# Optimization experiments

Hardware: AMD Instinct MI355X
Metric: run time of the kernel (lower is better)

The kernel has to match this reference:

```python
import jax, jax.numpy as jnp
import numpy as np

N_NODES = 100000
N_EDGES = 3200000
N_FEAT = 128
N_GRAPHS = 512
BN_EPS = 1e-5


def setup_inputs() -> dict:
    key = jax.random.key(0)
    ks = jax.random.split(key, 16)
    x = jax.random.normal(ks[0], (N_NODES, N_FEAT), dtype=jnp.float32)
    edge_index = jax.random.randint(ks[1], (2, N_EDGES), 0, N_NODES, dtype=jnp.int32)
    batch = jnp.sort(jax.random.randint(ks[2], (N_NODES,), 0, N_GRAPHS, dtype=jnp.int32))
    def lin(k, fi, fo):
        s = 1.0 / np.sqrt(fi)
        return jax.random.uniform(k, (fi, fo), jnp.float32, -s, s)
    return {
        "x": x,
        "edge_index": edge_index,
        "batch": batch,
        # conv1: GraphConv(128 -> 30): lin_rel (with bias) + lin_root (no bias)
        "W_rel1": lin(ks[3], N_FEAT, 30),
        "W_root1": lin(ks[4], N_FEAT, 30),
        "b1": jnp.zeros((30,), jnp.float32),
        "bn1_g": jnp.ones((30,), jnp.float32),
        "bn1_b": jnp.zeros((30,), jnp.float32),
        "bn1_m": jnp.zeros((30,), jnp.float32),
        "bn1_v": jnp.ones((30,), jnp.float32),
        # conv2: GraphConv(30 -> 20)
        "W_rel2": lin(ks[5], 30, 20),
        "W_root2": lin(ks[6], 30, 20),
        "b2": jnp.zeros((20,), jnp.float32),
        "bn2_g": jnp.ones((20,), jnp.float32),
        "bn2_b": jnp.zeros((20,), jnp.float32),
        "bn2_m": jnp.zeros((20,), jnp.float32),
        "bn2_v": jnp.ones((20,), jnp.float32),
        # head
        "W_lin1": lin(ks[7], 40, 10),
        "b_lin1": jnp.zeros((10,), jnp.float32),
        "W_lin2": lin(ks[8], 10, 1),
        "b_lin2": jnp.zeros((1,), jnp.float32),
    }


def _bn(h, g, b, m, v):
    return (h - m) * jax.lax.rsqrt(v + BN_EPS) * g + b


def reference(x, edge_index, batch,
              W_rel1, W_root1, b1, bn1_g, bn1_b, bn1_m, bn1_v,
              W_rel2, W_root2, b2, bn2_g, bn2_b, bn2_m, bn2_v,
              W_lin1, b_lin1, W_lin2, b_lin2):
    n = x.shape[0]
    src, dst = edge_index[0], edge_index[1]
    # ---- GraphConv 1: out = aggr_add(x_src -> dst) @ W_rel + x @ W_root + b
    agg = jax.ops.segment_sum(x[src], dst, num_segments=n)  # [N,128]
    h = jax.nn.relu(agg @ W_rel1 + x @ W_root1 + b1)        # [N,30]
    h = _bn(h, bn1_g, bn1_b, bn1_m, bn1_v)
    # ---- GraphConv 2
    agg2 = jax.ops.segment_sum(h[src], dst, num_segments=n)  # [N,30]
    h2 = jax.nn.relu(agg2 @ W_rel2 + h @ W_root2 + b2)       # [N,20]
    h2 = _bn(h2, bn2_g, bn2_b, bn2_m, bn2_v)
    # ---- global pools over graph ids
    gmax = jax.ops.segment_max(h2, batch, num_segments=N_GRAPHS)  # [G,20]
    gmax = jnp.where(jnp.isfinite(gmax), gmax, 0.0)
    gsum = jax.ops.segment_sum(h2, batch, num_segments=N_GRAPHS)
    cnt = jax.ops.segment_sum(jnp.ones((n,), h2.dtype), batch, num_segments=N_GRAPHS)
    gmean = gsum / jnp.maximum(cnt, 1.0)[:, None]
    z = jnp.concatenate([gmax, gmean], axis=1)               # [G,40]
    z = jax.nn.relu(z @ W_lin1 + b_lin1)
    return jax.nn.sigmoid(z @ W_lin2 + b_lin2)               # [G,1]
```

## Files before the change

kernel.cpp:

```cpp
#include <hip/hip_runtime.h>
#include <math.h>

#define NFEAT 128
#define F1    30
#define F1P   32
#define F2    20

#define EPB   8192
#define BW    512
#define EDCAP 9216

__global__ __launch_bounds__(256) void k_prepw(
    const float* __restrict__ Wrel, const float* __restrict__ Wroot,
    float* __restrict__ Wp)
{
    int i = blockIdx.x * 256 + threadIdx.x;
    if (i >= 2 * 128 * 32) return;
    int table = i >> 12, rem = i & 4095, k = rem >> 5, j = rem & 31;
    const float* W = table ? Wroot : Wrel;
    Wp[i] = (j < F1) ? W[k * F1 + j] : 0.f;
}

__global__ __launch_bounds__(512) void k_proj1(
    const float* __restrict__ x, const float* __restrict__ Wp,
    float* __restrict__ y1, float* __restrict__ r1, int n)
{
    __shared__ float4 xs4[2048];
    int tid = threadIdx.x;
    int base = blockIdx.x * 64;

#pragma unroll
    for (int it = 0; it < 4; it++) {
        int idx = it * 512 + tid;
        int k4 = idx & 31, row = idx >> 5;
        int gnode = base + row;
        float4 v = make_float4(0.f, 0.f, 0.f, 0.f);
        if (gnode < n) v = ((const float4*)(x + (size_t)gnode * NFEAT))[k4];
        xs4[k4 * 64 + (row ^ k4)] = v;
    }
    __syncthreads();

    int lane = tid & 63;
    int combo = __builtin_amdgcn_readfirstlane(tid >> 6);
    int table = combo >> 2, q = combo & 3;
    int node = base + lane;
    if (node >= n) return;

    const float* Wt = Wp + table * 4096 + q * 8;
    float acc[8];
#pragma unroll
    for (int j = 0; j < 8; j++) acc[j] = 0.f;

    for (int k4 = 0; k4 < 32; k4++) {
        float4 xk = xs4[k4 * 64 + (lane ^ k4)];
#pragma unroll
        for (int kk = 0; kk < 4; kk++) {
            float xs = kk == 0 ? xk.x : kk == 1 ? xk.y : kk == 2 ? xk.z : xk.w;
            const float* w = Wt + (k4 * 4 + kk) * 32;
            acc[0] += xs * w[0]; acc[1] += xs * w[1];
            acc[2] += xs * w[2]; acc[3] += xs * w[3];
            acc[4] += xs * w[4]; acc[5] += xs * w[5];
            acc[6] += xs * w[6]; acc[7] += xs * w[7];
        }
    }
    float* outp = (table ? r1 : y1) + (size_t)node * F1P + q * 8;
    ((float4*)outp)[0] = make_float4(acc[0], acc[1], acc[2], acc[3]);
    ((float4*)outp)[1] = make_float4(acc[4], acc[5], acc[6], acc[7]);
}

__global__ __launch_bounds__(512) void k_p1(
    const int* __restrict__ ei, int* __restrict__ blockCnt,
    int E, int nbuck)
{
    __shared__ int lh[256];
    int t = threadIdx.x;
    for (int i = t; i < 256; i += 512) lh[i] = 0;
    __syncthreads();
    const int* dst = ei + E;
    int base = blockIdx.x * EPB;
#pragma unroll 4
    for (int k = 0; k < EPB / 512; k++) {
        int e = base + k * 512 + t;
        if (e < E) atomicAdd(&lh[dst[e] >> 9], 1);
    }
    __syncthreads();
    int* out = blockCnt + (size_t)blockIdx.x * nbuck;
    for (int i = t; i < nbuck; i += 512) out[i] = lh[i];
}

__global__ __launch_bounds__(256) void k_p2(
    const int* __restrict__ blockCnt, int* __restrict__ blockOff,
    int* __restrict__ bucketTot, int neb, int nbuck)
{
    __shared__ int sdata[256];
    __shared__ int carry_s;
    int b = blockIdx.x;
    int t = threadIdx.x;
    if (t == 0) carry_s = 0;
    __syncthreads();
    for (int base = 0; base < neb; base += 512) {
        int i0 = base + 2 * t, i1 = i0 + 1;
        int c0 = (i0 < neb) ? blockCnt[(size_t)i0 * nbuck + b] : 0;
        int c1 = (i1 < neb) ? blockCnt[(size_t)i1 * nbuck + b] : 0;
        int s = c0 + c1;
        sdata[t] = s;
        __syncthreads();
        for (int off = 1; off < 256; off <<= 1) {
            int tmp = (t >= off) ? sdata[t - off] : 0;
            __syncthreads();
            sdata[t] += tmp;
            __syncthreads();
        }
        int ex = carry_s + sdata[t] - s;
        if (i0 < neb) blockOff[(size_t)i0 * nbuck + b] = ex;
        if (i1 < neb) blockOff[(size_t)i1 * nbuck + b] = ex + c0;
        __syncthreads();
        if (t == 255) carry_s += sdata[255];
        __syncthreads();
    }
    if (t == 0) bucketTot[b] = carry_s;
}

__global__ __launch_bounds__(256) void k_p3(
    const int* __restrict__ bucketTot, int* __restrict__ bucketStart, int nbuck)
{
    __shared__ int sdata[256];
    int t = threadIdx.x;
    int v[4]; int s = 0;
#pragma unroll
    for (int i = 0; i < 4; i++) {
        int idx = t * 4 + i;
        v[i] = (idx < nbuck) ? bucketTot[idx] : 0;
        s += v[i];
    }
    sdata[t] = s;
    __syncthreads();
    for (int off = 1; off < 256; off <<= 1) {
        int tmp = (t >= off) ? sdata[t - off] : 0;
        __syncthreads();
        sdata[t] += tmp;
        __syncthreads();
    }
    int ex = sdata[t] - s;
#pragma unroll
    for (int i = 0; i < 4; i++) {
        int idx = t * 4 + i;
        if (idx < nbuck) bucketStart[idx] = ex;
        ex += v[i];
    }
    if (t == 255) bucketStart[nbuck] = sdata[255];
}

__global__ __launch_bounds__(512) void k_p4(
    const int* __restrict__ ei, const int* __restrict__ bucketStart,
    const int* __restrict__ blockOff, int* __restrict__ ebuf,
    int E, int nbuck)
{
    __shared__ int cur[256];
    int t = threadIdx.x;
    const int* boff = blockOff + (size_t)blockIdx.x * nbuck;
    for (int i = t; i < nbuck; i += 512) cur[i] = bucketStart[i] + boff[i];
    __syncthreads();
    const int* dst = ei + E;
    int base = blockIdx.x * EPB;
#pragma unroll 4
    for (int k = 0; k < EPB / 512; k++) {
        int e = base + k * 512 + t;
        if (e < E) {
            int s = ei[e], d = dst[e];
            int p = atomicAdd(&cur[d >> 9], 1);
            ebuf[p] = (s << 9) | (d & 511);
        }
    }
}

__global__ __launch_bounds__(512) void k_p6(
    const int* __restrict__ ebuf, const int* __restrict__ bucketStart,
    int* __restrict__ perm, int* __restrict__ deg, int* __restrict__ rowstart,
    int n, int t1, int t2, int t3)
{
    __shared__ int ed2[EDCAP];
    __shared__ int hist[1024];
    __shared__ int sdata[512];
    __shared__ int m0_s;
    int t = threadIdx.x;
    int b = blockIdx.x >> 1;
    int h = blockIdx.x & 1;
    int lo = bucketStart[b], hi = bucketStart[b + 1];
    hist[t] = 0; hist[t + 512] = 0;
    if (t == 0) m0_s = 0;
    __syncthreads();

    int c0 = 0;
    for (int p = lo + t; p < hi; p += 512) {
        int e = ebuf[p];
        int dl9 = e & 511;
        if ((dl9 >> 8) == 0) c0++;
        if ((dl9 >> 8) == h) {
            int src = e >> 9;
            int qq = (src >= t1) + (src >= t2) + (src >= t3);
            atomicAdd(&hist[(dl9 & 255) * 4 + qq], 1);
        }
    }
    atomicAdd(&m0_s, c0);
    __syncthreads();

    int v0 = hist[2 * t], v1 = hist[2 * t + 1];
    int ps = v0 + v1;
    sdata[t] = ps;
    __syncthreads();
    for (int off = 1; off < 512; off <<= 1) {
        int tmp = (t >= off) ? sdata[t - off] : 0;
        __syncthreads();
        sdata[t] += tmp;
        __syncthreads();
    }
    int ex = sdata[t] - ps;
    hist[2 * t] = ex;
    hist[2 * t + 1] = ex + v0;
    __syncthreads();
    int mh = sdata[511];
    int base = lo + (h ? m0_s : 0);

    if (t < 256) {
        int node = b * BW + h * 256 + t;
        if (node < n) {
            int s0 = hist[t * 4];
            int s1 = (t == 255) ? mh : hist[(t + 1) * 4];
            deg[node] = s1 - s0;
            rowstart[node] = base + s0;
        }
    }
    __syncthreads();

    for (int p = lo + t; p < hi; p += 512) {
        int e = ebuf[p];
        int dl9 = e & 511;
        if ((dl9 >> 8) == h) {
            int src = e >> 9;
            int qq = (src >= t1) + (src >= t2) + (src >= t3);
            int pos = atomicAdd(&hist[(dl9 & 255) * 4 + qq], 1);
            if (pos < EDCAP) ed2[pos] = src;
            else perm[base + pos] = src;
        }
    }
    __syncthreads();

    int mw = min(mh, EDCAP);
    for (int i = t; i < mw; i += 512) perm[base + i] = ed2[i];
}

__global__ __launch_bounds__(256) void k_agg1(
    const int* __restrict__ rowstart, const int* __restrict__ deg,
    const int* __restrict__ perm, const float* __restrict__ y1,
    float* __restrict__ agg1, int n)
{
    int idx = blockIdx.x * 256 + threadIdx.x;
    int node = idx >> 3, q = idx & 7;
    if (node >= n) return;
    int s = rowstart[node], e = s + deg[node];
    float4 acc = {0.f, 0.f, 0.f, 0.f};
    int j = s;
    for (; j + 8 <= e; j += 8) {
        int myp = perm[j + q];
#pragma unroll
        for (int k = 0; k < 8; k++) {
            int sr = __shfl(myp, k, 8);
            float4 v = *(const float4*)(y1 + (size_t)sr * F1P + q * 4);
            acc.x += v.x; acc.y += v.y; acc.z += v.z; acc.w += v.w;
        }
    }
    for (; j < e; j++) {
        int sr = perm[j];
        float4 v = *(const float4*)(y1 + (size_t)sr * F1P + q * 4);
        acc.x += v.x; acc.y += v.y; acc.z += v.z; acc.w += v.w;
    }
    *(float4*)(agg1 + (size_t)node * F1P + q * 4) = acc;
}

__global__ __launch_bounds__(256) void k_agg2(
    const int* __restrict__ rowstart, const int* __restrict__ deg,
    const int* __restrict__ perm, const float* __restrict__ y2,
    float* __restrict__ agg2, int n)
{
    int idx = blockIdx.x * 256 + threadIdx.x;
    int node = idx >> 3, q = idx & 7;
    if (node >= n) return;
    bool valid = (q < 5);
    int s = rowstart[node], e = s + deg[node];
    float4 acc = {0.f, 0.f, 0.f, 0.f};
    int j = s;
    for (; j + 8 <= e; j += 8) {
        int myp = perm[j + q];
#pragma unroll
        for (int k = 0; k < 8; k++) {
            int sr = __shfl(myp, k, 8);
            if (valid) {
                float4 v = *(const float4*)(y2 + (size_t)sr * F2 + q * 4);
                acc.x += v.x; acc.y += v.y; acc.z += v.z; acc.w += v.w;
            }
        }
    }
    if (valid) {
        for (; j < e; j++) {
            int sr = perm[j];
            float4 v = *(const float4*)(y2 + (size_t)sr * F2 + q * 4);
            acc.x += v.x; acc.y += v.y; acc.z += v.z; acc.w += v.w;
        }
        *(float4*)(agg2 + (size_t)node * F2 + q * 4) = acc;
    }
}

__global__ __launch_bounds__(256) void k_mid(
    const float* __restrict__ agg1, const float* __restrict__ r1,
    const float* __restrict__ b1,
    const float* __restrict__ g1, const float* __restrict__ bb1,
    const float* __restrict__ m1, const float* __restrict__ v1,
    const float* __restrict__ Wrel2, const float* __restrict__ Wroot2,
    const float* __restrict__ b2,
    float* __restrict__ y2, float* __restrict__ r2, int n)
{
    int node = blockIdx.x * 256 + threadIdx.x;
    if (node >= n) return;
    float h[F1];
    const float4* av = (const float4*)(agg1 + (size_t)node * F1P);
    const float4* rv = (const float4*)(r1   + (size_t)node * F1P);
#pragma unroll
    for (int q = 0; q < 8; q++) {
        float4 a = av[q], r = rv[q];
        int j = q * 4;
        if (j + 0 < F1) h[j + 0] = a.x + r.x;
        if (j + 1 < F1) h[j + 1] = a.y + r.y;
        if (j + 2 < F1) h[j + 2] = a.z + r.z;
        if (j + 3 < F1) h[j + 3] = a.w + r.w;
    }
#pragma unroll
    for (int j = 0; j < F1; j++) {
        float t = fmaxf(h[j] + b1[j], 0.f);
        float sc = g1[j] / sqrtf(v1[j] + 1e-5f);
        h[j] = (t - m1[j]) * sc + bb1[j];
    }
    float ay[F2], ar[F2];
#pragma unroll
    for (int j = 0; j < F2; j++) { ay[j] = 0.f; ar[j] = b2[j]; }
    for (int k = 0; k < F1; k++) {
        float hk = h[k];
#pragma unroll
        for (int j = 0; j < F2; j++) {
            ay[j] += hk * Wrel2 [k * F2 + j];
            ar[j] += hk * Wroot2[k * F2 + j];
        }
    }
    float4* yo = (float4*)(y2 + (size_t)node * F2);
    float4* ro = (float4*)(r2 + (size_t)node * F2);
#pragma unroll
    for (int q = 0; q < 5; q++) {
        float4 vy, vr;
        vy.x = ay[q*4+0]; vy.y = ay[q*4+1]; vy.z = ay[q*4+2]; vy.w = ay[q*4+3];
        vr.x = ar[q*4+0]; vr.y = ar[q*4+1]; vr.z = ar[q*4+2]; vr.w = ar[q*4+3];
        yo[q] = vy;  ro[q] = vr;
    }
}

__global__ __launch_bounds__(256) void k_pool(
    const float* __restrict__ agg2, const float* __restrict__ r2,
    const int* __restrict__ batch,
    const float* __restrict__ g2, const float* __restrict__ bb2,
    const float* __restrict__ m2, const float* __restrict__ v2,
    unsigned* __restrict__ gmaxU, float* __restrict__ gsum,
    int* __restrict__ cnt, int n)
{
    int t = threadIdx.x;
    if (t >= 240) return;
    int i = t / 20, j = t - (t / 20) * 20;
    int base = blockIdx.x * 256;
    int nend = min(base + 256, n);
    float sc = g2[j] / sqrtf(v2[j] + 1e-5f);
    float mj = m2[j], bj = bb2[j];

    int curg = -1, c = 0;
    float mx = -3.4e38f, sm = 0.f;
    for (int node = base + i; node < nend; node += 12) {
        int g = batch[node];
        if (g != curg) {
            if (curg >= 0) {
                atomicAdd(&gsum[curg * F2 + j], sm);
                unsigned bits = __float_as_uint(mx);
                unsigned mapped = (bits & 0x80000000u) ? ~bits : (bits | 0x80000000u);
                atomicMax(&gmaxU[curg * F2 + j], mapped);
                if (j == 0) atomicAdd(&cnt[curg], c);
            }
            curg = g; c = 0; mx = -3.4e38f; sm = 0.f;
        }
        float a = agg2[(size_t)node * F2 + j] + r2[(size_t)node * F2 + j];
        a = fmaxf(a, 0.f);
        float h2 = (a - mj) * sc + bj;
        mx = fmaxf(mx, h2); sm += h2; c++;
    }
    if (curg >= 0) {
        atomicAdd(&gsum[curg * F2 + j], sm);
        unsigned bits = __float_as_uint(mx);
        unsigned mapped = (bits & 0x80000000u) ? ~bits : (bits | 0x80000000u);
        atomicMax(&gmaxU[curg * F2 + j], mapped);
        if (j == 0) atomicAdd(&cnt[curg], c);
    }
}

__global__ __launch_bounds__(256) void k_head(
    const unsigned* __restrict__ gmaxU, const float* __restrict__ gsum,
    const int* __restrict__ cnt,
    const float* __restrict__ W1, const float* __restrict__ b1h,
    const float* __restrict__ W2, const float* __restrict__ b2h,
    float* __restrict__ out, int G)
{
    int g = blockIdx.x * 256 + threadIdx.x;
    if (g >= G) return;
    int c = cnt[g];
    float cf = fmaxf((float)c, 1.f);
    float z[2 * F2];
#pragma unroll
    for (int j = 0; j < F2; j++) {
        unsigned u = gmaxU[g * F2 + j];
        float gm = 0.f;
        if (c != 0) {
            gm = (u & 0x80000000u) ? __uint_as_float(u & 0x7FFFFFFFu)
                                   : __uint_as_float(~u);
            if (!isfinite(gm)) gm = 0.f;
        }
        z[j]      = gm;
        z[F2 + j] = gsum[g * F2 + j] / cf;
    }
    float a[10];
#pragma unroll
    for (int i = 0; i < 10; i++) a[i] = b1h[i];
    for (int k = 0; k < 2 * F2; k++) {
        float zk = z[k];
#pragma unroll
        for (int i = 0; i < 10; i++) a[i] += zk * W1[k * 10 + i];
    }
    float o = b2h[0];
#pragma unroll
    for (int i = 0; i < 10; i++) o += fmaxf(a[i], 0.f) * W2[i];
    out[g] = 1.f / (1.f + expf(-o));
}

extern "C" void kernel_launch(void* const* d_in, const int* in_sizes, int n_in,
                              void* d_out, int out_size, void* d_ws, size_t ws_size,
                              hipStream_t stream)
{
    const float* x      = (const float*)d_in[0];
    const int*   ei     = (const int*)  d_in[1];
    const int*   batch  = (const int*)  d_in[2];
    const float* Wrel1  = (const float*)d_in[3];
    const float* Wroot1 = (const float*)d_in[4];
    const float* b1     = (const float*)d_in[5];
    const float* bn1_g  = (const float*)d_in[6];
    const float* bn1_b  = (const float*)d_in[7];
    const float* bn1_m  = (const float*)d_in[8];
    const float* bn1_v  = (const float*)d_in[9];
    const float* Wrel2  = (const float*)d_in[10];
    const float* Wroot2 = (const float*)d_in[11];
    const float* b2     = (const float*)d_in[12];
    const float* bn2_g  = (const float*)d_in[13];
    const float* bn2_b  = (const float*)d_in[14];
    const float* bn2_m  = (const float*)d_in[15];
    const float* bn2_v  = (const float*)d_in[16];
    const float* W_lin1 = (const float*)d_in[17];
    const float* b_lin1 = (const float*)d_in[18];
    const float* W_lin2 = (const float*)d_in[19];
    const float* b_lin2 = (const float*)d_in[20];
    float* out = (float*)d_out;

    int n = in_sizes[0] / NFEAT;
    int E = in_sizes[1] / 2;
    int G = out_size;
    int nbuck = (n + BW - 1) / BW;
    int neb = (E + EPB - 1) / EPB;
    int qs = (n + 3) >> 2;

    char* p = (char*)d_ws;
    float* y1   = (float*)p;  p += (size_t)n * F1P * 4;
    float* r1   = (float*)p;  p += (size_t)n * F1P * 4;
    char* alias0 = p;
    float* agg1 = (float*)p;  p += (size_t)n * F1P * 4;
    float* y2   = (float*)p;  p += (size_t)n * F2 * 4;
    float* r2   = (float*)p;  p += (size_t)n * F2 * 4;
    char* alias1 = p;
    float* agg2 = (float*)p;  p += (size_t)n * F2 * 4;
    unsigned* gmaxU = (unsigned*)p;  p += (size_t)G * F2 * 4;
    float*    gsum  = (float*)p;     p += (size_t)G * F2 * 4;
    int*      cnt   = (int*)p;       p += (size_t)G * 4;
    int* deg      = (int*)p;  p += (size_t)n * 4;
    int* rowstart = (int*)p;  p += (size_t)n * 4;
    int* perm     = (int*)p;  p += (size_t)E * 4;
    float* Wp     = (float*)p; p += 2 * 128 * 32 * 4;

    int* ebuf = (int*)alias0;
    int* blockCnt    = (int*)alias1;
    int* blockOff    = blockCnt + (size_t)neb * nbuck;
    int* bucketTot   = blockOff + (size_t)neb * nbuck;
    int* bucketStart = bucketTot + nbuck;

    hipMemsetAsync(gmaxU, 0, (size_t)G * (F2 * 4 * 2 + 4), stream);

    k_p1<<<neb, 512, 0, stream>>>(ei, blockCnt, E, nbuck);
    k_p2<<<nbuck, 256, 0, stream>>>(blockCnt, blockOff, bucketTot, neb, nbuck);
    k_p3<<<1, 256, 0, stream>>>(bucketTot, bucketStart, nbuck);
    k_p4<<<neb, 512, 0, stream>>>(ei, bucketStart, blockOff, ebuf, E, nbuck);
    k_p6<<<nbuck * 2, 512, 0, stream>>>(ebuf, bucketStart, perm, deg, rowstart, n,
                                        qs, 2 * qs, 3 * qs);

    k_prepw<<<32, 256, 0, stream>>>(Wrel1, Wroot1, Wp);
    k_proj1<<<(n + 63) / 64, 512, 0, stream>>>(x, Wp, y1, r1, n);
    k_agg1<<<((size_t)n * 8 + 255) / 256, 256, 0, stream>>>(rowstart, deg, perm, y1, agg1, n);
    k_mid<<<(n + 255) / 256, 256, 0, stream>>>(agg1, r1, b1, bn1_g, bn1_b, bn1_m,
                                               bn1_v, Wrel2, Wroot2, b2, y2, r2, n);
    k_agg2<<<((size_t)n * 8 + 255) / 256, 256, 0, stream>>>(rowstart, deg, perm, y2, agg2, n);
    k_pool<<<(n + 255) / 256, 256, 0, stream>>>(agg2, r2, batch, bn2_g, bn2_b,
                                                bn2_m, bn2_v, gmaxU, gsum, cnt, n);
    k_head<<<(G + 255) / 256, 256, 0, stream>>>(gmaxU, gsum, cnt, W_lin1, b_lin1,
                                                W_lin2, b_lin2, out, G);
}
```

Baseline: 389.2 us.

## Fuse layer-1 aggregation with mid MLP and layer-2 aggregation with pooling

Merges the first neighbor aggregation with the BN/ReLU and second projection into one kernel using shared memory, and merges the second aggregation with BN and graph pooling. This removes the agg1/agg2 intermediate buffers and two launches, avoiding global round-trips of the aggregated features. The workspace layout is reorganized so ebuf and the bucket counters no longer alias the removed buffers. Pooling now runs serially on 20 threads per 32-node block, which issues more atomics per graph than the old 256-node blocks.

Result: faster. 366.5 us (-5.8%).

```diff
diff --git a/kernel.cpp b/kernel.cpp
--- a/kernel.cpp
+++ b/kernel.cpp
@@ -250,159 +250,200 @@
     for (int i = t; i < mw; i += 512) perm[base + i] = ed2[i];
 }
 
-__global__ __launch_bounds__(256) void k_agg1(
+__global__ __launch_bounds__(256) void k_agg1m(
     const int* __restrict__ rowstart, const int* __restrict__ deg,
     const int* __restrict__ perm, const float* __restrict__ y1,
-    float* __restrict__ agg1, int n)
-{
-    int idx = blockIdx.x * 256 + threadIdx.x;
-    int node = idx >> 3, q = idx & 7;
-    if (node >= n) return;
-    int s = rowstart[node], e = s + deg[node];
-    float4 acc = {0.f, 0.f, 0.f, 0.f};
-    int j = s;
-    for (; j + 8 <= e; j += 8) {
-        int myp = perm[j + q];
-#pragma unroll
-        for (int k = 0; k < 8; k++) {
-            int sr = __shfl(myp, k, 8);
-            float4 v = *(const float4*)(y1 + (size_t)sr * F1P + q * 4);
-            acc.x += v.x; acc.y += v.y; acc.z += v.z; acc.w += v.w;
-        }
-    }
-    for (; j < e; j++) {
-        int sr = perm[j];
-        float4 v = *(const float4*)(y1 + (size_t)sr * F1P + q * 4);
-        acc.x += v.x; acc.y += v.y; acc.z += v.z; acc.w += v.w;
-    }
-    *(float4*)(agg1 + (size_t)node * F1P + q * 4) = acc;
-}
-
-__global__ __launch_bounds__(256) void k_agg2(
-    const int* __restrict__ rowstart, const int* __restrict__ deg,
-    const int* __restrict__ perm, const float* __restrict__ y2,
-    float* __restrict__ agg2, int n)
-{
-    int idx = blockIdx.x * 256 + threadIdx.x;
-    int node = idx >> 3, q = idx & 7;
-    if (node >= n) return;
-    bool valid = (q < 5);
-    int s = rowstart[node], e = s + deg[node];
-    float4 acc = {0.f, 0.f, 0.f, 0.f};
-    int j = s;
-    for (; j + 8 <= e; j += 8) {
-        int myp = perm[j + q];
-#pragma unroll
-        for (int k = 0; k < 8; k++) {
-            int sr = __shfl(myp, k, 8);
-            if (valid) {
-                float4 v = *(const float4*)(y2 + (size_t)sr * F2 + q * 4);
-                acc.x += v.x; acc.y += v.y; acc.z += v.z; acc.w += v.w;
-            }
-        }
-    }
-    if (valid) {
-        for (; j < e; j++) {
-            int sr = perm[j];
-            float4 v = *(const float4*)(y2 + (size_t)sr * F2 + q * 4);
-            acc.x += v.x; acc.y += v.y; acc.z += v.z; acc.w += v.w;
-        }
-        *(float4*)(agg2 + (size_t)node * F2 + q * 4) = acc;
-    }
-}
-
-__global__ __launch_bounds__(256) void k_mid(
-    const float* __restrict__ agg1, const float* __restrict__ r1,
-    const float* __restrict__ b1,
-    const float* __restrict__ g1, const float* __restrict__ bb1,
-    const float* __restrict__ m1, const float* __restrict__ v1,
+    const float* __restrict__ r1,
+    const float* __restrict__ b1, const float* __restrict__ g1,
+    const float* __restrict__ bb1, const float* __restrict__ m1,
+    const float* __restrict__ v1,
     const float* __restrict__ Wrel2, const float* __restrict__ Wroot2,
     const float* __restrict__ b2,
     float* __restrict__ y2, float* __restrict__ r2, int n)
 {
-    int node = blockIdx.x * 256 + threadIdx.x;
-    if (node >= n) return;
-    float h[F1];
-    const float4* av = (const float4*)(agg1 + (size_t)node * F1P);
-    const float4* rv = (const float4*)(r1   + (size_t)node * F1P);
-#pragma unroll
-    for (int q = 0; q < 8; q++) {
-        float4 a = av[q], r = rv[q];
-        int j = q * 4;
-        if (j + 0 < F1) h[j + 0] = a.x + r.x;
-        if (j + 1 < F1) h[j + 1] = a.y + r.y;
-        if (j + 2 < F1) h[j + 2] = a.z + r.z;
-        if (j + 3 < F1) h[j + 3] = a.w + r.w;
-    }
-#pragma unroll
-    for (int j = 0; j < F1; j++) {
-        float t = fmaxf(h[j] + b1[j], 0.f);
-        float sc = g1[j] / sqrtf(v1[j] + 1e-5f);
-        h[j] = (t - m1[j]) * sc + bb1[j];
-    }
-    float ay[F2], ar[F2];
-#pragma unroll
-    for (int j = 0; j < F2; j++) { ay[j] = 0.f; ar[j] = b2[j]; }
-    for (int k = 0; k < F1; k++) {
-        float hk = h[k];
-#pragma unroll
-        for (int j = 0; j < F2; j++) {
-            ay[j] += hk * Wrel2 [k * F2 + j];
-            ar[j] += hk * Wroot2[k * F2 + j];
-        }
-    }
-    float4* yo = (float4*)(y2 + (size_t)node * F2);
-    float4* ro = (float4*)(r2 + (size_t)node * F2);
-#pragma unroll
-    for (int q = 0; q < 5; q++) {
-        float4 vy, vr;
-        vy.x = ay[q*4+0]; vy.y = ay[q*4+1]; vy.z = ay[q*4+2]; vy.w = ay[q*4+3];
-        vr.x = ar[q*4+0]; vr.y = ar[q*4+1]; vr.z = ar[q*4+2]; vr.w = ar[q*4+3];
-        yo[q] = vy;  ro[q] = vr;
-    }
-}
-
-__global__ __launch_bounds__(256) void k_pool(
-    const float* __restrict__ agg2, const float* __restrict__ r2,
-    const int* __restrict__ batch,
+    __shared__ float sAcc[32][33];
+    __shared__ float sH[32][31];
+    __shared__ float sW[30][40];
+    __shared__ float sP[4][30];
+    __shared__ float sB2[20];
+    int t = threadIdx.x;
+    int base = blockIdx.x * 32;
+    int nl = t >> 3, q = t & 7;
+    int node = base + nl;
+
+    if (t < 30) {
+        sP[0][t] = b1[t];
+        sP[1][t] = g1[t] / sqrtf(v1[t] + 1e-5f);
+        sP[2][t] = m1[t];
+        sP[3][t] = bb1[t];
+    }
+    if (t >= 32 && t < 52) sB2[t - 32] = b2[t - 32];
+    for (int i = t; i < 1200; i += 256) {
+        int k = i / 40, o = i - k * 40;
+        sW[k][o] = (o < 20) ? Wrel2[k * 20 + o] : Wroot2[k * 20 + (o - 20)];
+    }
+
+    float4 acc = {0.f, 0.f, 0.f, 0.f};
+    if (node < n) {
+        int s = rowstart[node], e = s + deg[node];
+        int j = s;
+        for (; j + 8 <= e; j += 8) {
+            int myp = perm[j + q];
+#pragma unroll
+            for (int k = 0; k < 8; k++) {
+                int sr = __shfl(myp, k, 8);
+                float4 v = *(const float4*)(y1 + (size_t)sr * F1P + q * 4);
+                acc.x += v.x; acc.y += v.y; acc.z += v.z; acc.w += v.w;
+            }
+        }
+        for (; j < e; j++) {
+            int sr = perm[j];
+            float4 v = *(const float4*)(y1 + (size_t)sr * F1P + q * 4);
+            acc.x += v.x; acc.y += v.y; acc.z += v.z; acc.w += v.w;
+        }
+    }
+    sAcc[nl][q * 4 + 0] = acc.x; sAcc[nl][q * 4 + 1] = acc.y;
+    sAcc[nl][q * 4 + 2] = acc.z; sAcc[nl][q * 4 + 3] = acc.w;
+    __syncthreads();
+
+    for (int w = t; w < 960; w += 256) {
+        int wl = w / 30, k = w - wl * 30;
+        int nd = base + wl;
+        if (nd < n) {
+            float a = sAcc[wl][k] + r1[(size_t)nd * F1P + k] + sP[0][k];
+            a = fmaxf(a, 0.f);
+            sH[wl][k] = (a - sP[2][k]) * sP[1][k] + sP[3][k];
+        }
+    }
+    __syncthreads();
+
+    if (node < n) {
+        int ob = q * 5;
+        bool isroot = (ob >= 20);
+        float o0 = 0.f, o1 = 0.f, o2 = 0.f, o3 = 0.f, o4 = 0.f;
+        if (isroot) {
+            o0 = sB2[ob - 20]; o1 = sB2[ob - 19]; o2 = sB2[ob - 18];
+            o3 = sB2[ob - 17]; o4 = sB2[ob - 16];
+        }
+        for (int k = 0; k < 30; k++) {
+            float hk = sH[nl][k];
+            o0 += hk * sW[k][ob + 0];
+            o1 += hk * sW[k][ob + 1];
+            o2 += hk * sW[k][ob + 2];
+            o3 += hk * sW[k][ob + 3];
+            o4 += hk * sW[k][ob + 4];
+        }
+        float* dst = isroot ? (r2 + (size_t)node * F2 + (ob - 20))
+                            : (y2 + (size_t)node * F2 + ob);
+        dst[0] = o0; dst[1] = o1; dst[2] = o2; dst[3] = o3; dst[4] = o4;
+    }
+}
+
+__global__ __launch_bounds__(256) void k_agg2p(
+    const int* __restrict__ rowstart, const int* __restrict__ deg,
+    const int* __restrict__ perm, const float* __restrict__ y2,
+    const float* __restrict__ r2, const int* __restrict__ batch,
     const float* __restrict__ g2, const float* __restrict__ bb2,
     const float* __restrict__ m2, const float* __restrict__ v2,
     unsigned* __restrict__ gmaxU, float* __restrict__ gsum,
     int* __restrict__ cnt, int n)
 {
-    int t = threadIdx.x;
-    if (t >= 240) return;
-    int i = t / 20, j = t - (t / 20) * 20;
-    int base = blockIdx.x * 256;
-    int nend = min(base + 256, n);
-    float sc = g2[j] / sqrtf(v2[j] + 1e-5f);
-    float mj = m2[j], bj = bb2[j];
-
-    int curg = -1, c = 0;
-    float mx = -3.4e38f, sm = 0.f;
-    for (int node = base + i; node < nend; node += 12) {
-        int g = batch[node];
-        if (g != curg) {
-            if (curg >= 0) {
-                atomicAdd(&gsum[curg * F2 + j], sm);
-                unsigned bits = __float_as_uint(mx);
-                unsigned mapped = (bits & 0x80000000u) ? ~bits : (bits | 0x80000000u);
-                atomicMax(&gmaxU[curg * F2 + j], mapped);
-                if (j == 0) atomicAdd(&cnt[curg], c);
+    __shared__ float sAcc[32][21];
+    __shared__ float sH[32][21];
+    __shared__ float sSc[20], sM[20], sBb[20];
+    __shared__ int   sB[32];
+    int t = threadIdx.x;
+    int base = blockIdx.x * 32;
+    int nl = t >> 3, q = t & 7;
+    int node = base + nl;
+
+    if (t < 20) {
+        sSc[t] = g2[t] / sqrtf(v2[t] + 1e-5f);
+        sM[t]  = m2[t];
+    }
+    if (t >= 32 && t < 52) sBb[t - 32] = bb2[t - 32];
+    if (t >= 64 && t < 96) {
+        int nd = base + (t - 64);
+        sB[t - 64] = (nd < n) ? batch[nd] : -1;
+    }
+
+    bool valid = (q < 5);
+    float4 acc = {0.f, 0.f, 0.f, 0.f};
+    if (node < n) {
+        int s = rowstart[node], e = s + deg[node];
+        int j = s;
+        for (; j + 8 <= e; j += 8) {
+            int myp = perm[j + q];
+#pragma unroll
+            for (int k = 0; k < 8; k++) {
+                int sr = __shfl(myp, k, 8);
+                if (valid) {
+                    float4 v = *(const float4*)(y2 + (size_t)sr * F2 + q * 4);
+                    acc.x += v.x; acc.y += v.y; acc.z += v.z; acc.w += v.w;
+                }
             }
-            curg = g; c = 0; mx = -3.4e38f; sm = 0.f;
-        }
-        float a = agg2[(size_t)node * F2 + j] + r2[(size_t)node * F2 + j];
-        a = fmaxf(a, 0.f);
-        float h2 = (a - mj) * sc + bj;
-        mx = fmaxf(mx, h2); sm += h2; c++;
-    }
-    if (curg >= 0) {
-        atomicAdd(&gsum[curg * F2 + j], sm);
-        unsigned bits = __float_as_uint(mx);
-        unsigned mapped = (bits & 0x80000000u) ? ~bits : (bits | 0x80000000u);
-        atomicMax(&gmaxU[curg * F2 + j], mapped);
-        if (j == 0) atomicAdd(&cnt[curg], c);
+        }
+        if (valid) {
+            for (; j < e; j++) {
+                int sr = perm[j];
+                float4 v = *(const float4*)(y2 + (size_t)sr * F2 + q * 4);
+                acc.x += v.x; acc.y += v.y; acc.z += v.z; acc.w += v.w;
+            }
+        }
+    }
+    if (valid && node < n) {
+        sAcc[nl][q * 4 + 0] = acc.x; sAcc[nl][q * 4 + 1] = acc.y;
+        sAcc[nl][q * 4 + 2] = acc.z; sAcc[nl][q * 4 + 3] = acc.w;
+    }
+    __syncthreads();
+
+    for (int w = t; w < 640; w += 256) {
+        int wl = w / 20, f = w - wl * 20;
+        int nd = base + wl;
+        if (nd < n) {
+            float a = sAcc[wl][f] + r2[(size_t)nd * F2 + f];
+            a = fmaxf(a, 0.f);
+            sH[wl][f] = (a - sM[f]) * sSc[f] + sBb[f];
+        }
+    }
+    __syncthreads();
+
+    if (t < 20) {
+        int f = t;
+        int curg = -1; float sm = 0.f, mx = -3.4e38f;
+        for (int wl = 0; wl < 32; wl++) {
+            int g = sB[wl];
+            if (g < 0) break;
+            if (g != curg) {
+                if (curg >= 0) {
+                    atomicAdd(&gsum[curg * F2 + f], sm);
+                    unsigned bits = __float_as_uint(mx);
+                    unsigned mp = (bits & 0x80000000u) ? ~bits : (bits | 0x80000000u);
+                    atomicMax(&gmaxU[curg * F2 + f], mp);
+                }
+                curg = g; sm = 0.f; mx = -3.4e38f;
+            }
+            float h2 = sH[wl][f];
+            sm += h2; mx = fmaxf(mx, h2);
+        }
+        if (curg >= 0) {
+            atomicAdd(&gsum[curg * F2 + f], sm);
+            unsigned bits = __float_as_uint(mx);
+            unsigned mp = (bits & 0x80000000u) ? ~bits : (bits | 0x80000000u);
+            atomicMax(&gmaxU[curg * F2 + f], mp);
+        }
+    } else if (t == 20) {
+        int curg = -1, c = 0;
+        for (int wl = 0; wl < 32; wl++) {
+            int g = sB[wl];
+            if (g < 0) break;
+            if (g != curg) {
+                if (curg >= 0) atomicAdd(&cnt[curg], c);
+                curg = g; c = 0;
+            }
+            c++;
+        }
+        if (curg >= 0) atomicAdd(&cnt[curg], c);
     }
 }
 
@@ -481,25 +522,20 @@
     char* p = (char*)d_ws;
     float* y1   = (float*)p;  p += (size_t)n * F1P * 4;
     float* r1   = (float*)p;  p += (size_t)n * F1P * 4;
-    char* alias0 = p;
-    float* agg1 = (float*)p;  p += (size_t)n * F1P * 4;
     float* y2   = (float*)p;  p += (size_t)n * F2 * 4;
     float* r2   = (float*)p;  p += (size_t)n * F2 * 4;
-    char* alias1 = p;
-    float* agg2 = (float*)p;  p += (size_t)n * F2 * 4;
+    int*   ebuf = (int*)p;    p += (size_t)E * 4;
+    int*   perm = (int*)p;    p += (size_t)E * 4;
+    int* deg      = (int*)p;  p += (size_t)n * 4;
+    int* rowstart = (int*)p;  p += (size_t)n * 4;
+    int* blockCnt    = (int*)p;  p += (size_t)neb * nbuck * 4;
+    int* blockOff    = (int*)p;  p += (size_t)neb * nbuck * 4;
+    int* bucketTot   = (int*)p;  p += (size_t)nbuck * 4;
+    int* bucketStart = (int*)p;  p += (size_t)(nbuck + 1) * 4;
     unsigned* gmaxU = (unsigned*)p;  p += (size_t)G * F2 * 4;
     float*    gsum  = (float*)p;     p += (size_t)G * F2 * 4;
     int*      cnt   = (int*)p;       p += (size_t)G * 4;
-    int* deg      = (int*)p;  p += (size_t)n * 4;
-    int* rowstart = (int*)p;  p += (size_t)n * 4;
-    int* perm     = (int*)p;  p += (size_t)E * 4;
-    float* Wp     = (float*)p; p += 2 * 128 * 32 * 4;
-
-    int* ebuf = (int*)alias0;
-    int* blockCnt    = (int*)alias1;
-    int* blockOff    = blockCnt + (size_t)neb * nbuck;
-    int* bucketTot   = blockOff + (size_t)neb * nbuck;
-    int* bucketStart = bucketTot + nbuck;
+    float* Wp       = (float*)p;     p += 2 * 128 * 32 * 4;
 
     hipMemsetAsync(gmaxU, 0, (size_t)G * (F2 * 4 * 2 + 4), stream);
 
@@ -512,12 +548,12 @@
 
     k_prepw<<<32, 256, 0, stream>>>(Wrel1, Wroot1, Wp);
     k_proj1<<<(n + 63) / 64, 512, 0, stream>>>(x, Wp, y1, r1, n);
-    k_agg1<<<((size_t)n * 8 + 255) / 256, 256, 0, stream>>>(rowstart, deg, perm, y1, agg1, n);
-    k_mid<<<(n + 255) / 256, 256, 0, stream>>>(agg1, r1, b1, bn1_g, bn1_b, bn1_m,
-                                               bn1_v, Wrel2, Wroot2, b2, y2, r2, n);
-    k_agg2<<<((size_t)n * 8 + 255) / 256, 256, 0, stream>>>(rowstart, deg, perm, y2, agg2, n);
-    k_pool<<<(n + 255) / 256, 256, 0, stream>>>(agg2, r2, batch, bn2_g, bn2_b,
-                                                bn2_m, bn2_v, gmaxU, gsum, cnt, n);
+    k_agg1m<<<(n + 31) / 32, 256, 0, stream>>>(rowstart, deg, perm, y1, r1,
+                                               b1, bn1_g, bn1_b, bn1_m, bn1_v,
+                                               Wrel2, Wroot2, b2, y2, r2, n);
+    k_agg2p<<<(n + 31) / 32, 256, 0, stream>>>(rowstart, deg, perm, y2, r2, batch,
+                                               bn2_g, bn2_b, bn2_m, bn2_v,
+                                               gmaxU, gsum, cnt, n);
     k_head<<<(G + 255) / 256, 256, 0, stream>>>(gmaxU, gsum, cnt, W_lin1, b_lin1,
                                                 W_lin2, b_lin2, out, G);
 }
```
